# Performance work log

Measured on AMD Instinct MI355X. Metric: run time of the kernel, lower is better.

Reference implementation:

```python
import jax, jax.numpy as jnp
import numpy as np


def setup_inputs() -> dict:
    key = jax.random.key(0)
    ks = jax.random.split(key, 5)
    B, Lq, Lkv, E, H = 4, 4096, 4096, 1024, 128
    x = jax.random.normal(ks[0], (B, Lq, E), dtype=jnp.float32)
    z = jax.random.normal(ks[1], (B, Lkv, E), dtype=jnp.float32)
    s = 1.0 / np.sqrt(E)
    Wq = jax.random.normal(ks[2], (H, E), dtype=jnp.float32) * s
    Wk = jax.random.normal(ks[3], (H, E), dtype=jnp.float32) * s
    Wv = jax.random.normal(ks[4], (H, E), dtype=jnp.float32) * s
    return {"x": x, "z": z, "Wq": Wq, "Wk": Wk, "Wv": Wv}


def reference(x, z, Wq, Wk, Wv):
    # q: [B, Lq, H]; k, v: [B, Lkv, H]  (torch Linear: y = x @ W.T)
    q = jnp.einsum('bqe,he->bqh', x, Wq)
    k = jnp.einsum('bke,he->bkh', z, Wk)
    v = jnp.einsum('bke,he->bkh', z, Wv)
    # NOTE: original code MULTIPLIES by sqrt(head_dim) (faithful reproduction)
    scale = jnp.asarray(k.shape[-1], x.dtype) ** 0.5
    weights = jnp.einsum('bqh,bkh->bqk', q, k) * scale  # [B, Lq, Lkv]
    weights = jax.nn.softmax(weights, axis=-1)
    logits = jnp.einsum('bqk,bkh->bqh', weights, v)  # [B, Lq, H]
    return logits
```

## Files before the change

kernel.cpp:

```cpp
#include <hip/hip_runtime.h>

typedef __attribute__((ext_vector_type(8))) short short8;
typedef __attribute__((ext_vector_type(4))) float f32x4;
typedef __attribute__((ext_vector_type(4))) float float4v;
typedef __attribute__((ext_vector_type(4))) unsigned int u32x4;
typedef unsigned int __attribute__((may_alias)) u32ma;

#define B_   4
#define LQ   4096
#define LKV  4096
#define E_   1024
#define H_   128
#define NSPLIT 4
#define KVSPL (LKV / NSPLIT)
#define NT    (KVSPL / 64)
#define WELEM (H_ * E_)

static __device__ __forceinline__ unsigned short bf16_rne(float f) {
    unsigned int u = __float_as_uint(f);
    u += 0x7fffu + ((u >> 16) & 1u);
    return (unsigned short)(u >> 16);
}
static __device__ __forceinline__ float bf16_tof(unsigned short h) {
    return __uint_as_float(((unsigned int)h) << 16);
}
static __device__ __forceinline__ f32x4 mfma16(short8 a, short8 b, f32x4 c) {
    return __builtin_amdgcn_mfma_f32_16x16x32_bf16(a, b, c, 0, 0, 0);
}
static __device__ __forceinline__ void gload16(const unsigned short* g, unsigned short* l) {
    __builtin_amdgcn_global_load_lds(
        (const __attribute__((address_space(1))) unsigned int*)g,
        (__attribute__((address_space(3))) unsigned int*)l, 16, 0, 0);
}

__global__ __launch_bounds__(256) void convert_w_kernel(
    const float* __restrict__ Wq, const float* __restrict__ Wk, const float* __restrict__ Wv,
    unsigned short* __restrict__ wqh, unsigned short* __restrict__ wql,
    unsigned short* __restrict__ wkh, unsigned short* __restrict__ wkl,
    unsigned short* __restrict__ wvh)
{
    const int kb = blockIdx.x;
    const int which = blockIdx.y;
    const float* W = (which == 0) ? Wq : (which == 1) ? Wk : Wv;
    unsigned short* outh = (which == 0) ? wqh : (which == 1) ? wkh : wvh;
    unsigned short* outl = (which == 0) ? wql : wkl;
    const int t = threadIdx.x;
#pragma unroll
    for (int i = 0; i < 4; ++i) {
        const int c = t * 4 + i;
        const int h = c >> 3;
        const int k = kb * 64 + (((c & 7) ^ (h & 7)) * 8);
        const float* src = W + (size_t)h * E_ + k;
        float4v v0 = *(const float4v*)(src);
        float4v v1 = *(const float4v*)(src + 4);
        short8 hi, lo;
#pragma unroll
        for (int e = 0; e < 4; ++e) {
            unsigned short h0 = bf16_rne(v0[e]);
            unsigned short h1 = bf16_rne(v1[e]);
            hi[e] = (short)h0; hi[e + 4] = (short)h1;
            lo[e] = (short)bf16_rne(v0[e] - bf16_tof(h0));
            lo[e + 4] = (short)bf16_rne(v1[e] - bf16_tof(h1));
        }
        *(short8*)&outh[(size_t)kb * 8192 + (size_t)c * 8] = hi;
        if (which < 2) *(short8*)&outl[(size_t)kb * 8192 + (size_t)c * 8] = lo;
    }
}

__global__ __launch_bounds__(512, 1) void proj_kernel(
    const float* __restrict__ x, const float* __restrict__ z,
    const unsigned short* __restrict__ wqh, const unsigned short* __restrict__ wql,
    const unsigned short* __restrict__ wkh, const unsigned short* __restrict__ wkl,
    const unsigned short* __restrict__ wvh,
    unsigned short* __restrict__ qhi, unsigned short* __restrict__ qlo,
    unsigned short* __restrict__ khi, unsigned short* __restrict__ klo,
    unsigned short* __restrict__ vt)
{
    const int bid = blockIdx.x;
    const bool qmode = bid < 128;
    const int m0 = (qmode ? bid : bid - 128) * 128;
    const float* Asrc = qmode ? x : z;
    const unsigned short* W1h = qmode ? wqh : wkh;
    const unsigned short* W1l = qmode ? wql : wkl;

    const int t = threadIdx.x;
    const int w = t >> 6, l = t & 63, lg = (l >> 4) & 3, ll = l & 15;
    const int mw = w & 3, nw = w >> 2;

    __shared__ unsigned short Ah[8192];
    __shared__ unsigned short Al[8192];
    __shared__ unsigned short Wh[2][8192];
    __shared__ unsigned short Wl[2][8192];
    __shared__ unsigned short Wv2[2][8192];

    const int ar = t >> 2, aq = t & 3;
    float4v ra[4];
    auto loadA = [&](int e0) {
        const float* p = Asrc + (size_t)(m0 + ar) * E_ + e0 + aq * 16;
#pragma unroll
        for (int i = 0; i < 4; ++i) ra[i] = *(const float4v*)(p + i * 4);
    };
    auto writeA = [&]() {
#pragma unroll
        for (int half = 0; half < 2; ++half) {
            short8 hi, lo;
#pragma unroll
            for (int e = 0; e < 4; ++e) {
                float v0 = ra[2 * half][e];
                float v1 = ra[2 * half + 1][e];
                unsigned short h0 = bf16_rne(v0);
                unsigned short h1 = bf16_rne(v1);
                hi[e] = (short)h0; hi[e + 4] = (short)h1;
                lo[e] = (short)bf16_rne(v0 - bf16_tof(h0));
                lo[e + 4] = (short)bf16_rne(v1 - bf16_tof(h1));
            }
            const int j = 2 * aq + half;
            const int off = ar * 64 + ((j ^ (ar & 7)) * 8);
            *(short8*)&Ah[off] = hi;
            *(short8*)&Al[off] = lo;
        }
    };
    auto issueW = [&](int kb, int bsel) {
#pragma unroll
        for (int i = 0; i < 2; ++i) {
            const int cbase = w * 128 + i * 64;
            const size_t so = (size_t)kb * 8192 + (size_t)(cbase + l) * 8;
            gload16(W1h + so, &Wh[bsel][(size_t)cbase * 8]);
            gload16(W1l + so, &Wl[bsel][(size_t)cbase * 8]);
            if (!qmode) gload16(wvh + so, &Wv2[bsel][(size_t)cbase * 8]);
        }
    };

    f32x4 acc[2][4], accv[2][4];
    const f32x4 zz = {0.f, 0.f, 0.f, 0.f};
#pragma unroll
    for (int rf = 0; rf < 2; ++rf)
#pragma unroll
        for (int cf = 0; cf < 4; ++cf) { acc[rf][cf] = zz; accv[rf][cf] = zz; }

    issueW(0, 0);
    loadA(0);
    writeA();
    __syncthreads();

    for (int kb = 0; kb < 16; ++kb) {
        const int bsel = kb & 1;
        if (kb < 15) { issueW(kb + 1, bsel ^ 1); loadA((kb + 1) * 64); }

#pragma unroll
        for (int ks = 0; ks < 2; ++ks) {
            short8 a_h[2], a_l[2];
#pragma unroll
            for (int rf = 0; rf < 2; ++rf) {
                const int r = mw * 32 + rf * 16 + ll;
                const int off = r * 64 + (((ks * 4 + lg) ^ (ll & 7)) * 8);
                a_h[rf] = *(const short8*)&Ah[off];
                a_l[rf] = *(const short8*)&Al[off];
            }
#pragma unroll
            for (int cf = 0; cf < 4; ++cf) {
                const int hrow = nw * 64 + cf * 16 + ll;
                const int off = hrow * 64 + (((ks * 4 + lg) ^ (ll & 7)) * 8);
                short8 bh = *(const short8*)&Wh[bsel][off];
                short8 bl = *(const short8*)&Wl[bsel][off];
#pragma unroll
                for (int rf = 0; rf < 2; ++rf) {
                    acc[rf][cf] = mfma16(a_h[rf], bh, acc[rf][cf]);
                    acc[rf][cf] = mfma16(a_h[rf], bl, acc[rf][cf]);
                    acc[rf][cf] = mfma16(a_l[rf], bh, acc[rf][cf]);
                }
                if (!qmode) {
                    short8 bv = *(const short8*)&Wv2[bsel][off];
#pragma unroll
                    for (int rf = 0; rf < 2; ++rf)
                        accv[rf][cf] = mfma16(a_h[rf], bv, accv[rf][cf]);
                }
            }
        }
        __syncthreads();
        if (kb < 15) {
            writeA();
            __syncthreads();
        }
    }

#pragma unroll
    for (int rf = 0; rf < 2; ++rf)
#pragma unroll
        for (int cf = 0; cf < 4; ++cf)
#pragma unroll
            for (int j = 0; j < 4; ++j) {
                const int m = m0 + mw * 32 + rf * 16 + 4 * lg + j;
                const int h = nw * 64 + cf * 16 + ll;
                const float val = acc[rf][cf][j];
                unsigned short hi = bf16_rne(val);
                unsigned short lo = bf16_rne(val - bf16_tof(hi));
                const size_t o = (size_t)m * H_ + h;
                if (qmode) {
                    qhi[o] = hi; qlo[o] = lo;
                } else {
                    khi[o] = hi; klo[o] = lo;
                    const int b = m >> 12, kv = m & 4095;
                    const int kv5 = kv & 31;
                    const int kvp = (kv & ~31) | (((kv5 >> 2) & 3) << 3)
                                  | (((kv5 >> 4) & 1) << 2) | (kv5 & 3);
                    vt[(size_t)b * ((size_t)H_ * LKV) + (size_t)h * LKV + kvp] =
                        bf16_rne(accv[rf][cf][j]);
                }
            }
}

__global__ __launch_bounds__(256, 2) void attn_kernel(
    const unsigned short* __restrict__ qhi, const unsigned short* __restrict__ qlo,
    const unsigned short* __restrict__ khi, const unsigned short* __restrict__ klo,
    const unsigned short* __restrict__ vt,
    float* __restrict__ Opart, float* __restrict__ msb, float* __restrict__ lsb)
{
    const int blk = blockIdx.x;
    const int bb = blk & 3;
    const int qt = (blk >> 2) & 31;
    const int split = blk >> 7;
    const int t = threadIdx.x;
    const int w = t >> 6, l = t & 63, lg = (l >> 4) & 3, ll = l & 15;

    __shared__ unsigned short Kh[2][8192];
    __shared__ unsigned short Kl[2][8192];
    __shared__ unsigned short Vb[8192];

    const float CSC = 11.313708498984761f * 1.4426950408889634f;

    short8 qh[2][4], ql[2][4];
#pragma unroll
    for (int b = 0; b < 2; ++b) {
        const size_t qrow = (size_t)(bb * LQ + qt * 128 + w * 32 + b * 16 + ll) * H_;
#pragma unroll
        for (int ks = 0; ks < 4; ++ks) {
            qh[b][ks] = *(const short8*)(qhi + qrow + ks * 32 + lg * 8);
            ql[b][ks] = *(const short8*)(qlo + qrow + ks * 32 + lg * 8);
        }
    }

    const int kv_base = split * KVSPL;
    const unsigned short* khb = khi + (size_t)bb * LKV * H_;
    const unsigned short* klb = klo + (size_t)bb * LKV * H_;
    const unsigned short* vbg = vt + (size_t)bb * ((size_t)H_ * LKV);

    auto issue_K = [&](int kv0, int sel) {
#pragma unroll
        for (int ci = 0; ci < 4; ++ci) {
            const int chunk = w * 4 + ci;
            const int row = chunk * 4 + (l >> 4);
            const int c = l & 15;
            const size_t so = (size_t)(kv0 + row) * H_ + ((c ^ (row & 7)) * 8);
            gload16(khb + so, &Kh[sel][chunk * 512]);
            gload16(klb + so, &Kl[sel][chunk * 512]);
        }
    };
    auto issue_V = [&](int kv0) {
#pragma unroll
        for (int ci = 0; ci < 4; ++ci) {
            const int chunk = w * 4 + ci;
            const int row = chunk * 8 + (l >> 3);
            const int c = l & 7;
            gload16(vbg + (size_t)row * LKV + kv0 + ((c ^ (row & 7)) * 8),
                    &Vb[chunk * 512]);
        }
    };

    f32x4 O[8][2];
    const f32x4 zz = {0.f, 0.f, 0.f, 0.f};
#pragma unroll
    for (int f = 0; f < 8; ++f) { O[f][0] = zz; O[f][1] = zz; }
    float mold[2] = {-1e30f, -1e30f};
    float lsum[2] = {0.f, 0.f};

    issue_K(kv_base, 0);
    issue_V(kv_base);
    asm volatile("s_waitcnt vmcnt(0)" ::: "memory");
    __builtin_amdgcn_s_barrier();

    for (int ti = 0; ti < NT; ++ti) {
        const int cur = ti & 1;
        if (ti + 1 < NT) issue_K(kv_base + (ti + 1) * 64, cur ^ 1);
        __builtin_amdgcn_sched_barrier(0);

        f32x4 S[4][2];
#pragma unroll
        for (int a = 0; a < 4; ++a) { S[a][0] = zz; S[a][1] = zz; }
        __builtin_amdgcn_s_setprio(1);
#pragma unroll
        for (int ks = 0; ks < 4; ++ks) {
#pragma unroll
            for (int a = 0; a < 4; ++a) {
                const int row = a * 16 + ll;
                const int off = row * 128 + (((ks * 4 + lg) ^ (ll & 7)) * 8);
                short8 kh  = *(const short8*)&Kh[cur][off];
                short8 kl2 = *(const short8*)&Kl[cur][off];
                S[a][0] = mfma16(kh,  qh[0][ks], S[a][0]);
                S[a][0] = mfma16(kh,  ql[0][ks], S[a][0]);
                S[a][0] = mfma16(kl2, qh[0][ks], S[a][0]);
                S[a][1] = mfma16(kh,  qh[1][ks], S[a][1]);
                S[a][1] = mfma16(kh,  ql[1][ks], S[a][1]);
                S[a][1] = mfma16(kl2, qh[1][ks], S[a][1]);
            }
        }
        __builtin_amdgcn_s_setprio(0);

        unsigned int pw[2][8];
#pragma unroll
        for (int b = 0; b < 2; ++b) {
            float ma0 = fmaxf(fmaxf(S[0][b][0], S[0][b][1]), fmaxf(S[0][b][2], S[0][b][3]));
            float ma1 = fmaxf(fmaxf(S[1][b][0], S[1][b][1]), fmaxf(S[1][b][2], S[1][b][3]));
            float ma2 = fmaxf(fmaxf(S[2][b][0], S[2][b][1]), fmaxf(S[2][b][2], S[2][b][3]));
            float ma3 = fmaxf(fmaxf(S[3][b][0], S[3][b][1]), fmaxf(S[3][b][2], S[3][b][3]));
            float mx = fmaxf(fmaxf(ma0, ma1), fmaxf(ma2, ma3));
            mx = fmaxf(mx, __shfl_xor(mx, 16));
            mx = fmaxf(mx, __shfl_xor(mx, 32));
            const float mxs = mx * CSC;
            const bool need = !__all(mxs <= mold[b]);
            const float mn = need ? fmaxf(mold[b], mxs) : mold[b];
            float ps = 0.f;
#pragma unroll
            for (int a = 0; a < 4; ++a) {
                float p0 = exp2f(fmaf(S[a][b][0], CSC, -mn));
                float p1 = exp2f(fmaf(S[a][b][1], CSC, -mn));
                float p2 = exp2f(fmaf(S[a][b][2], CSC, -mn));
                float p3 = exp2f(fmaf(S[a][b][3], CSC, -mn));
                ps += (p0 + p1) + (p2 + p3);
                unsigned int pk0, pk1;
                asm("v_cvt_pk_bf16_f32 %0, %1, %2" : "=v"(pk0) : "v"(p0), "v"(p1));
                asm("v_cvt_pk_bf16_f32 %0, %1, %2" : "=v"(pk1) : "v"(p2), "v"(p3));
                pw[b][2 * a]     = pk0;
                pw[b][2 * a + 1] = pk1;
            }
            ps += __shfl_xor(ps, 16);
            ps += __shfl_xor(ps, 32);
            if (need) {
                const float corr = exp2f(mold[b] - mn);
                lsum[b] = lsum[b] * corr + ps;
                mold[b] = mn;
#pragma unroll
                for (int f = 0; f < 8; ++f) O[f][b] *= corr;
            } else {
                lsum[b] += ps;
            }
        }

        asm volatile("s_waitcnt lgkmcnt(0)" ::: "memory");
        if (ti + 1 < NT) {
            asm volatile("s_waitcnt vmcnt(8)" ::: "memory");
        } else {
            asm volatile("s_waitcnt vmcnt(0)" ::: "memory");
        }
        __builtin_amdgcn_sched_barrier(0);
        __builtin_amdgcn_s_barrier();

        __builtin_amdgcn_s_setprio(1);
#pragma unroll
        for (int ks = 0; ks < 2; ++ks) {
            union { u32x4 u; short8 s; } pb0, pb1;
            pb0.u = (u32x4){pw[0][4 * ks], pw[0][4 * ks + 1], pw[0][4 * ks + 2], pw[0][4 * ks + 3]};
            pb1.u = (u32x4){pw[1][4 * ks], pw[1][4 * ks + 1], pw[1][4 * ks + 2], pw[1][4 * ks + 3]};
#pragma unroll
            for (int f = 0; f < 8; ++f) {
                const int row = f * 16 + ll;
                short8 va = *(const short8*)&Vb[row * 64
                                               + (((ks * 4 + lg) ^ (ll & 7)) * 8)];
                O[f][0] = mfma16(va, pb0.s, O[f][0]);
                O[f][1] = mfma16(va, pb1.s, O[f][1]);
            }
        }
        __builtin_amdgcn_s_setprio(0);

        asm volatile("s_waitcnt vmcnt(0) lgkmcnt(0)" ::: "memory");
        __builtin_amdgcn_sched_barrier(0);
        __builtin_amdgcn_s_barrier();

        if (ti + 1 < NT) issue_V(kv_base + (ti + 1) * 64);
        __builtin_amdgcn_sched_barrier(0);
    }

    const size_t obase = ((((size_t)split * 4 + bb) * 32 + qt) * 4 + w) * 16;
#pragma unroll
    for (int f = 0; f < 8; ++f)
#pragma unroll
        for (int b = 0; b < 2; ++b)
            *(float4v*)&Opart[(obase + f * 2 + b) * 256 + l * 4] = O[f][b];

    if (lg == 0) {
#pragma unroll
        for (int b = 0; b < 2; ++b) {
            const int q = qt * 128 + w * 32 + b * 16 + ll;
            msb[((size_t)split * 4 + bb) * LQ + q] = mold[b];
            lsb[((size_t)split * 4 + bb) * LQ + q] = lsum[b];
        }
    }
}

__global__ __launch_bounds__(512) void combine_kernel(
    const float* __restrict__ Opart, const float* __restrict__ msb,
    const float* __restrict__ lsb, float* __restrict__ out)
{
    const int blk = blockIdx.x;
    const int bb = blk & 3;
    const int qt = (blk >> 2) & 31;
    const int fg = blk >> 7;
    const int t = threadIdx.x;
    const int w = t >> 6, l = t & 63, lg = (l >> 4) & 3, ll = l & 15;
    const int wq = w & 3, wf = w >> 2;

#pragma unroll
    for (int b = 0; b < 2; ++b) {
        const int q = qt * 128 + wq * 32 + b * 16 + ll;
        float ms[NSPLIT], ls[NSPLIT];
#pragma unroll
        for (int s = 0; s < NSPLIT; ++s) {
            ms[s] = msb[((size_t)s * 4 + bb) * LQ + q];
            ls[s] = lsb[((size_t)s * 4 + bb) * LQ + q];
        }
        float mM = fmaxf(fmaxf(ms[0], ms[1]), fmaxf(ms[2], ms[3]));
        float wsp[NSPLIT];
        float L = 0.f;
#pragma unroll
        for (int s = 0; s < NSPLIT; ++s) {
            wsp[s] = exp2f(ms[s] - mM);
            L += ls[s] * wsp[s];
        }
        const float inv = 1.f / L;
#pragma unroll
        for (int fi = 0; fi < 2; ++fi) {
            const int f = fg * 4 + wf * 2 + fi;
            f32x4 acc = {0.f, 0.f, 0.f, 0.f};
#pragma unroll
            for (int s = 0; s < NSPLIT; ++s) {
                const size_t ob = ((((size_t)s * 4 + bb) * 32 + qt) * 4 + wq) * 16 + f * 2 + b;
                float4v ov = *(const float4v*)&Opart[ob * 256 + l * 4];
#pragma unroll
                for (int j = 0; j < 4; ++j) acc[j] += ov[j] * wsp[s];
            }
#pragma unroll
            for (int j = 0; j < 4; ++j) acc[j] *= inv;
            *(float4v*)&out[((size_t)bb * LQ + q) * H_ + f * 16 + lg * 4] = acc;
        }
    }
}

extern "C" void kernel_launch(void* const* d_in, const int* in_sizes, int n_in,
                              void* d_out, int out_size, void* d_ws, size_t ws_size,
                              hipStream_t stream) {
    const float* x  = (const float*)d_in[0];
    const float* z  = (const float*)d_in[1];
    const float* Wq = (const float*)d_in[2];
    const float* Wk = (const float*)d_in[3];
    const float* Wv = (const float*)d_in[4];
    float* out = (float*)d_out;

    const size_t NQ = (size_t)B_ * LQ * H_;
    unsigned short* qhi = (unsigned short*)d_ws;
    unsigned short* qlo = qhi + NQ;
    unsigned short* khi = qlo + NQ;
    unsigned short* klo = khi + NQ;
    unsigned short* vtp = klo + NQ;
    float* Opart = (float*)(vtp + NQ);
    float* msb   = Opart + (size_t)NSPLIT * NQ;
    float* lsb   = msb + (size_t)NSPLIT * B_ * LQ;
    unsigned short* wqh = (unsigned short*)(lsb + (size_t)NSPLIT * B_ * LQ);
    unsigned short* wql = wqh + WELEM;
    unsigned short* wkh = wql + WELEM;
    unsigned short* wkl = wkh + WELEM;
    unsigned short* wvh = wkl + WELEM;

    convert_w_kernel<<<dim3(16, 3), 256, 0, stream>>>(Wq, Wk, Wv, wqh, wql, wkh, wkl, wvh);
    proj_kernel<<<dim3(256), 512, 0, stream>>>(x, z, wqh, wql, wkh, wkl, wvh,
                                               qhi, qlo, khi, klo, vtp);
    attn_kernel<<<dim3(512), 256, 0, stream>>>(qhi, qlo, khi, klo, vtp, Opart, msb, lsb);
    combine_kernel<<<dim3(256), 512, 0, stream>>>(Opart, msb, lsb, out);
}
```

Before: 140.6 us.

## Software-pipeline QK^T of the next KV tile with softmax and PV of the current

The KV loop is restructured into a two-stage software pipeline. The QK^T MFMAs for tile i+1 are issued alongside the softmax and PV of tile i, using two ping-pong score register sets. Shared-memory buffers are rebalanced: K-hi and V are double-buffered and K-lo is single-buffered, with loads split into separate issue points. The goal is to hide softmax ALU latency and global loads behind matrix work. The cost is higher register pressure under the 2-waves/SIMD launch bound and more complex barrier placement.

Result: slower. 167.3 us (+19.0%).

```diff
diff --git a/kernel.cpp b/kernel.cpp
--- a/kernel.cpp
+++ b/kernel.cpp
@@ -224,8 +224,8 @@
     const int w = t >> 6, l = t & 63, lg = (l >> 4) & 3, ll = l & 15;
 
     __shared__ unsigned short Kh[2][8192];
-    __shared__ unsigned short Kl[2][8192];
-    __shared__ unsigned short Vb[8192];
+    __shared__ unsigned short Kl[8192];
+    __shared__ unsigned short Vb[2][8192];
 
     const float CSC = 11.313708498984761f * 1.4426950408889634f;
 
@@ -245,25 +245,34 @@
     const unsigned short* klb = klo + (size_t)bb * LKV * H_;
     const unsigned short* vbg = vt + (size_t)bb * ((size_t)H_ * LKV);
 
-    auto issue_K = [&](int kv0, int sel) {
+    auto issue_Kh = [&](int kv0, unsigned short* dst) {
 #pragma unroll
         for (int ci = 0; ci < 4; ++ci) {
             const int chunk = w * 4 + ci;
             const int row = chunk * 4 + (l >> 4);
             const int c = l & 15;
-            const size_t so = (size_t)(kv0 + row) * H_ + ((c ^ (row & 7)) * 8);
-            gload16(khb + so, &Kh[sel][chunk * 512]);
-            gload16(klb + so, &Kl[sel][chunk * 512]);
-        }
-    };
-    auto issue_V = [&](int kv0) {
+            gload16(khb + (size_t)(kv0 + row) * H_ + ((c ^ (row & 7)) * 8),
+                    dst + chunk * 512);
+        }
+    };
+    auto issue_Kl = [&](int kv0) {
+#pragma unroll
+        for (int ci = 0; ci < 4; ++ci) {
+            const int chunk = w * 4 + ci;
+            const int row = chunk * 4 + (l >> 4);
+            const int c = l & 15;
+            gload16(klb + (size_t)(kv0 + row) * H_ + ((c ^ (row & 7)) * 8),
+                    &Kl[chunk * 512]);
+        }
+    };
+    auto issue_V = [&](int kv0, unsigned short* dst) {
 #pragma unroll
         for (int ci = 0; ci < 4; ++ci) {
             const int chunk = w * 4 + ci;
             const int row = chunk * 8 + (l >> 3);
             const int c = l & 7;
             gload16(vbg + (size_t)row * LKV + kv0 + ((c ^ (row & 7)) * 8),
-                    &Vb[chunk * 512]);
+                    dst + chunk * 512);
         }
     };
 
@@ -273,29 +282,20 @@
     for (int f = 0; f < 8; ++f) { O[f][0] = zz; O[f][1] = zz; }
     float mold[2] = {-1e30f, -1e30f};
     float lsum[2] = {0.f, 0.f};
-
-    issue_K(kv_base, 0);
-    issue_V(kv_base);
-    asm volatile("s_waitcnt vmcnt(0)" ::: "memory");
-    __builtin_amdgcn_s_barrier();
-
-    for (int ti = 0; ti < NT; ++ti) {
-        const int cur = ti & 1;
-        if (ti + 1 < NT) issue_K(kv_base + (ti + 1) * 64, cur ^ 1);
-        __builtin_amdgcn_sched_barrier(0);
-
-        f32x4 S[4][2];
+    f32x4 SA[4][2], SB[4][2];
+    unsigned int pw[2][8];
+
+    auto qkt = [&](const unsigned short (&KhB)[8192], f32x4 (&S)[4][2]) {
 #pragma unroll
         for (int a = 0; a < 4; ++a) { S[a][0] = zz; S[a][1] = zz; }
-        __builtin_amdgcn_s_setprio(1);
 #pragma unroll
         for (int ks = 0; ks < 4; ++ks) {
 #pragma unroll
             for (int a = 0; a < 4; ++a) {
                 const int row = a * 16 + ll;
                 const int off = row * 128 + (((ks * 4 + lg) ^ (ll & 7)) * 8);
-                short8 kh  = *(const short8*)&Kh[cur][off];
-                short8 kl2 = *(const short8*)&Kl[cur][off];
+                short8 kh  = *(const short8*)&KhB[off];
+                short8 kl2 = *(const short8*)&Kl[off];
                 S[a][0] = mfma16(kh,  qh[0][ks], S[a][0]);
                 S[a][0] = mfma16(kh,  ql[0][ks], S[a][0]);
                 S[a][0] = mfma16(kl2, qh[0][ks], S[a][0]);
@@ -304,9 +304,9 @@
                 S[a][1] = mfma16(kl2, qh[1][ks], S[a][1]);
             }
         }
-        __builtin_amdgcn_s_setprio(0);
-
-        unsigned int pw[2][8];
+    };
+
+    auto softmax_step = [&](f32x4 (&S)[4][2]) {
 #pragma unroll
         for (int b = 0; b < 2; ++b) {
             float ma0 = fmaxf(fmaxf(S[0][b][0], S[0][b][1]), fmaxf(S[0][b][2], S[0][b][3]));
@@ -345,16 +345,9 @@
                 lsum[b] += ps;
             }
         }
-
-        asm volatile("s_waitcnt lgkmcnt(0)" ::: "memory");
-        if (ti + 1 < NT) {
-            asm volatile("s_waitcnt vmcnt(8)" ::: "memory");
-        } else {
-            asm volatile("s_waitcnt vmcnt(0)" ::: "memory");
-        }
-        __builtin_amdgcn_sched_barrier(0);
-        __builtin_amdgcn_s_barrier();
-
+    };
+
+    auto pv = [&](const unsigned short (&VbB)[8192]) {
         __builtin_amdgcn_s_setprio(1);
 #pragma unroll
         for (int ks = 0; ks < 2; ++ks) {
@@ -364,21 +357,68 @@
 #pragma unroll
             for (int f = 0; f < 8; ++f) {
                 const int row = f * 16 + ll;
-                short8 va = *(const short8*)&Vb[row * 64
-                                               + (((ks * 4 + lg) ^ (ll & 7)) * 8)];
+                short8 va = *(const short8*)&VbB[row * 64
+                                                + (((ks * 4 + lg) ^ (ll & 7)) * 8)];
                 O[f][0] = mfma16(va, pb0.s, O[f][0]);
                 O[f][1] = mfma16(va, pb1.s, O[f][1]);
             }
         }
         __builtin_amdgcn_s_setprio(0);
-
-        asm volatile("s_waitcnt vmcnt(0) lgkmcnt(0)" ::: "memory");
-        __builtin_amdgcn_sched_barrier(0);
-        __builtin_amdgcn_s_barrier();
-
-        if (ti + 1 < NT) issue_V(kv_base + (ti + 1) * 64);
-        __builtin_amdgcn_sched_barrier(0);
+    };
+
+#define BARRIER_X() do { \
+        asm volatile("s_waitcnt lgkmcnt(0)" ::: "memory"); \
+        __builtin_amdgcn_sched_barrier(0); \
+        __builtin_amdgcn_s_barrier(); } while (0)
+#define BARRIER_Y() do { \
+        asm volatile("s_waitcnt vmcnt(0) lgkmcnt(0)" ::: "memory"); \
+        __builtin_amdgcn_sched_barrier(0); \
+        __builtin_amdgcn_s_barrier(); } while (0)
+
+    issue_Kh(kv_base, &Kh[0][0]);
+    issue_Kl(kv_base);
+    issue_V(kv_base, &Vb[0][0]);
+    asm volatile("s_waitcnt vmcnt(0)" ::: "memory");
+    __builtin_amdgcn_s_barrier();
+
+    issue_Kh(kv_base + 64, &Kh[1][0]);
+    qkt(Kh[0], SA);
+    BARRIER_X();
+    issue_Kl(kv_base + 64);
+    BARRIER_Y();
+    issue_V(kv_base + 64, &Vb[1][0]);
+
+    for (int p = 0; p < 7; ++p) {
+        const int t1 = 2 * p + 1;
+        issue_Kh(kv_base + (t1 + 1) * 64, &Kh[0][0]);
+        qkt(Kh[1], SB);
+        softmax_step(SA);
+        BARRIER_X();
+        issue_Kl(kv_base + (t1 + 1) * 64);
+        pv(Vb[0]);
+        BARRIER_Y();
+        issue_V(kv_base + (t1 + 1) * 64, &Vb[0][0]);
+
+        issue_Kh(kv_base + (t1 + 2) * 64, &Kh[1][0]);
+        qkt(Kh[0], SA);
+        softmax_step(SB);
+        BARRIER_X();
+        issue_Kl(kv_base + (t1 + 2) * 64);
+        pv(Vb[1]);
+        BARRIER_Y();
+        issue_V(kv_base + (t1 + 2) * 64, &Vb[1][0]);
     }
+
+    qkt(Kh[1], SB);
+    softmax_step(SA);
+    BARRIER_X();
+    pv(Vb[0]);
+    BARRIER_Y();
+    softmax_step(SB);
+    pv(Vb[1]);
+
+#undef BARRIER_X
+#undef BARRIER_Y
 
     const size_t obase = ((((size_t)split * 4 + bb) * 32 + qt) * 4 + w) * 16;
 #pragma unroll
```

## Software-pipeline attention loop so QK^T of next tile overlaps PV of previous

Applied to the files above, without the earlier changes.

Restructures the KV tile loop into a two-stage software pipeline: QK^T for tile t+1 is computed while the PV product for tile t runs, with double-buffered probability registers (pwA/pwB) and an unrolled loop over tile pairs. V loads are issued later and waited on with partial vmcnt counts, so global loads overlap MFMA work. The aim is to hide the softmax and load latency between the two matmul phases. The cost is higher register pressure from two sets of P values, and the explicit setprio hints are dropped.

After: 146.1 us. 3.9% more time.

```diff
diff --git a/kernel.cpp b/kernel.cpp
--- a/kernel.cpp
+++ b/kernel.cpp
@@ -273,29 +273,20 @@
     for (int f = 0; f < 8; ++f) { O[f][0] = zz; O[f][1] = zz; }
     float mold[2] = {-1e30f, -1e30f};
     float lsum[2] = {0.f, 0.f};
-
-    issue_K(kv_base, 0);
-    issue_V(kv_base);
-    asm volatile("s_waitcnt vmcnt(0)" ::: "memory");
-    __builtin_amdgcn_s_barrier();
-
-    for (int ti = 0; ti < NT; ++ti) {
-        const int cur = ti & 1;
-        if (ti + 1 < NT) issue_K(kv_base + (ti + 1) * 64, cur ^ 1);
-        __builtin_amdgcn_sched_barrier(0);
-
-        f32x4 S[4][2];
+    f32x4 S[4][2];
+    unsigned int pwA[2][8], pwB[2][8];
+
+    auto qkt = [&](int sel) {
 #pragma unroll
         for (int a = 0; a < 4; ++a) { S[a][0] = zz; S[a][1] = zz; }
-        __builtin_amdgcn_s_setprio(1);
 #pragma unroll
         for (int ks = 0; ks < 4; ++ks) {
 #pragma unroll
             for (int a = 0; a < 4; ++a) {
                 const int row = a * 16 + ll;
                 const int off = row * 128 + (((ks * 4 + lg) ^ (ll & 7)) * 8);
-                short8 kh  = *(const short8*)&Kh[cur][off];
-                short8 kl2 = *(const short8*)&Kl[cur][off];
+                short8 kh  = *(const short8*)&Kh[sel][off];
+                short8 kl2 = *(const short8*)&Kl[sel][off];
                 S[a][0] = mfma16(kh,  qh[0][ks], S[a][0]);
                 S[a][0] = mfma16(kh,  ql[0][ks], S[a][0]);
                 S[a][0] = mfma16(kl2, qh[0][ks], S[a][0]);
@@ -304,9 +295,26 @@
                 S[a][1] = mfma16(kl2, qh[1][ks], S[a][1]);
             }
         }
-        __builtin_amdgcn_s_setprio(0);
-
-        unsigned int pw[2][8];
+    };
+
+    auto pv = [&](unsigned int (&pw)[2][8]) {
+#pragma unroll
+        for (int ks = 0; ks < 2; ++ks) {
+            union { u32x4 u; short8 s; } pb0, pb1;
+            pb0.u = (u32x4){pw[0][4 * ks], pw[0][4 * ks + 1], pw[0][4 * ks + 2], pw[0][4 * ks + 3]};
+            pb1.u = (u32x4){pw[1][4 * ks], pw[1][4 * ks + 1], pw[1][4 * ks + 2], pw[1][4 * ks + 3]};
+#pragma unroll
+            for (int f = 0; f < 8; ++f) {
+                const int row = f * 16 + ll;
+                short8 va = *(const short8*)&Vb[row * 64
+                                               + (((ks * 4 + lg) ^ (ll & 7)) * 8)];
+                O[f][0] = mfma16(va, pb0.s, O[f][0]);
+                O[f][1] = mfma16(va, pb1.s, O[f][1]);
+            }
+        }
+    };
+
+    auto softmax_step = [&](unsigned int (&pw)[2][8]) {
 #pragma unroll
         for (int b = 0; b < 2; ++b) {
             float ma0 = fmaxf(fmaxf(S[0][b][0], S[0][b][1]), fmaxf(S[0][b][2], S[0][b][3]));
@@ -345,40 +353,56 @@
                 lsum[b] += ps;
             }
         }
-
-        asm volatile("s_waitcnt lgkmcnt(0)" ::: "memory");
-        if (ti + 1 < NT) {
-            asm volatile("s_waitcnt vmcnt(8)" ::: "memory");
-        } else {
-            asm volatile("s_waitcnt vmcnt(0)" ::: "memory");
-        }
-        __builtin_amdgcn_sched_barrier(0);
-        __builtin_amdgcn_s_barrier();
-
-        __builtin_amdgcn_s_setprio(1);
-#pragma unroll
-        for (int ks = 0; ks < 2; ++ks) {
-            union { u32x4 u; short8 s; } pb0, pb1;
-            pb0.u = (u32x4){pw[0][4 * ks], pw[0][4 * ks + 1], pw[0][4 * ks + 2], pw[0][4 * ks + 3]};
-            pb1.u = (u32x4){pw[1][4 * ks], pw[1][4 * ks + 1], pw[1][4 * ks + 2], pw[1][4 * ks + 3]};
-#pragma unroll
-            for (int f = 0; f < 8; ++f) {
-                const int row = f * 16 + ll;
-                short8 va = *(const short8*)&Vb[row * 64
-                                               + (((ks * 4 + lg) ^ (ll & 7)) * 8)];
-                O[f][0] = mfma16(va, pb0.s, O[f][0]);
-                O[f][1] = mfma16(va, pb1.s, O[f][1]);
-            }
-        }
-        __builtin_amdgcn_s_setprio(0);
-
-        asm volatile("s_waitcnt vmcnt(0) lgkmcnt(0)" ::: "memory");
-        __builtin_amdgcn_sched_barrier(0);
-        __builtin_amdgcn_s_barrier();
-
-        if (ti + 1 < NT) issue_V(kv_base + (ti + 1) * 64);
-        __builtin_amdgcn_sched_barrier(0);
+    };
+
+#define WAIT_BAR(cntasm) do { \
+        asm volatile(cntasm ::: "memory"); \
+        __builtin_amdgcn_sched_barrier(0); \
+        __builtin_amdgcn_s_barrier(); } while (0)
+
+    issue_K(kv_base, 0);
+    WAIT_BAR("s_waitcnt vmcnt(0)");
+
+    issue_K(kv_base + 64, 1);
+    qkt(0);
+    softmax_step(pwA);
+    WAIT_BAR("s_waitcnt lgkmcnt(0)");
+    issue_V(kv_base + 0 * 64);
+    WAIT_BAR("s_waitcnt vmcnt(4)");
+
+#pragma unroll
+    for (int p = 0; p < 7; ++p) {
+        const int tA = 2 * p + 1;
+        issue_K(kv_base + (tA + 1) * 64, 0);
+        qkt(1);
+        WAIT_BAR("s_waitcnt vmcnt(8)");
+        pv(pwA);
+        softmax_step(pwB);
+        WAIT_BAR("s_waitcnt lgkmcnt(0)");
+        issue_V(kv_base + tA * 64);
+        WAIT_BAR("s_waitcnt vmcnt(4)");
+
+        const int tB = 2 * p + 2;
+        issue_K(kv_base + (tB + 1) * 64, 1);
+        qkt(0);
+        WAIT_BAR("s_waitcnt vmcnt(8)");
+        pv(pwB);
+        softmax_step(pwA);
+        WAIT_BAR("s_waitcnt lgkmcnt(0)");
+        issue_V(kv_base + tB * 64);
+        WAIT_BAR("s_waitcnt vmcnt(4)");
     }
+
+    qkt(1);
+    WAIT_BAR("s_waitcnt vmcnt(0)");
+    pv(pwA);
+    softmax_step(pwB);
+    WAIT_BAR("s_waitcnt lgkmcnt(0)");
+    issue_V(kv_base + 15 * 64);
+    WAIT_BAR("s_waitcnt vmcnt(0)");
+    pv(pwB);
+
+#undef WAIT_BAR
 
     const size_t obase = ((((size_t)split * 4 + bb) * 32 + qt) * 4 + w) * 16;
 #pragma unroll
```
